# Performance work log

Measured on AMD Instinct MI355X. Metric: run time of the kernel, lower is better.

## Reference

```python
import jax, jax.numpy as jnp
import numpy as np

B, S, D_MODEL, HEAD, D_KV = 8, 1024, 1024, 16, 64


def setup_inputs() -> dict:
    key = jax.random.key(0)
    ks = jax.random.split(key, 10)
    std = 1.0 / np.sqrt(D_MODEL)
    inp = {
        "queries": jax.random.normal(ks[0], (B, S, D_MODEL), jnp.float32),
        "keys": jax.random.normal(ks[1], (B, S, D_MODEL), jnp.float32),
        "values": jax.random.normal(ks[2], (B, S, D_MODEL), jnp.float32),
        "group_prob": jax.random.uniform(ks[3], (B, 1, S, S), jnp.float32),
        "attention_mask": jax.random.randint(ks[4], (B, 1, S, S), 0, 2, jnp.int32),
        "Wq": jax.random.normal(ks[5], (HEAD * D_KV, D_MODEL), jnp.float32) * std,
        "bq": jnp.zeros((HEAD * D_KV,), jnp.float32),
        "Wk": jax.random.normal(ks[6], (HEAD * D_KV, D_MODEL), jnp.float32) * std,
        "bk": jnp.zeros((HEAD * D_KV,), jnp.float32),
        "Wv": jax.random.normal(ks[7], (HEAD * D_KV, D_MODEL), jnp.float32) * std,
        "bv": jnp.zeros((HEAD * D_KV,), jnp.float32),
    }
    return inp


def reference(queries, keys, values, group_prob, attention_mask, Wq, bq, Wk, bk, Wv, bv):
    b, nq = queries.shape[:2]
    # QKV projections -> [b, head, seq, d_kv]
    q = (queries @ Wq.T + bq).reshape(b, nq, HEAD, D_KV).transpose(0, 2, 1, 3)
    k = (keys @ Wk.T + bk).reshape(b, -1, HEAD, D_KV).transpose(0, 2, 1, 3)
    v = (values @ Wv.T + bv).reshape(b, -1, HEAD, D_KV).transpose(0, 2, 1, 3)
    # scaled scores [b, head, nq, nk]
    att = jnp.einsum("bhqd,bhkd->bhqk", q, k) / np.sqrt(D_KV).astype(np.float32)
    # NOTE: the original torch code calls att.masked_fill(...) (out-of-place)
    # and discards the result, so attention_mask has no effect. Replicated here.
    att = jax.nn.softmax(att, axis=-1)
    att = att * group_prob  # post-softmax group scaling (breaks fused SDPA)
    out = jnp.einsum("bhqk,bhkd->bhqd", att, v)
    return out.transpose(0, 2, 1, 3).reshape(b, nq, HEAD * D_KV)
```

## Files before the change

### kernel.cpp

```cpp
#include <hip/hip_runtime.h>

#define B_SZ 8
#define S_SZ 1024
#define DM   1024
#define NH   16
#define DK   64

typedef __bf16 bf16;
typedef __bf16 bf16x8 __attribute__((ext_vector_type(8)));
typedef float  f32x4  __attribute__((ext_vector_type(4)));

__device__ __forceinline__ f32x4 mfma16x16x32(bf16x8 a, bf16x8 b, f32x4 c) {
    return __builtin_amdgcn_mfma_f32_16x16x32_bf16(a, b, c, 0, 0, 0);
}

typedef const __attribute__((address_space(1))) void* gptr_t;
typedef __attribute__((address_space(3))) void*       sptr_t;
__device__ __forceinline__ void async_cp16(const void* g, void* s) {
    __builtin_amdgcn_global_load_lds((gptr_t)g, (sptr_t)s, 16, 0, 0);
}

__global__ __launch_bounds__(256)
void cvt_kernel(const float* __restrict__ x0, const float* __restrict__ x1,
                const float* __restrict__ x2, const float* __restrict__ w0,
                const float* __restrict__ w1, const float* __restrict__ w2,
                bf16* __restrict__ xb, bf16* __restrict__ wb)
{
    const int z = blockIdx.y;
    const float* src;
    bf16* dst;
    int n;
    if (z < 3) {
        src = (z == 0) ? x0 : (z == 1) ? x1 : x2;
        dst = xb + (size_t)z * (8u * 1024 * 1024);
        n = 8 * 1024 * 1024;
    } else {
        const int w = z - 3;
        src = (w == 0) ? w0 : (w == 1) ? w1 : w2;
        dst = wb + (size_t)w * (1024 * 1024);
        n = 1024 * 1024;
    }
    const int idx = (blockIdx.x * 256 + threadIdx.x) * 8;
    if (idx >= n) return;
    const float4 a = *(const float4*)(src + idx);
    const float4 c = *(const float4*)(src + idx + 4);
    union { bf16 h[8]; uint4 u; } pk;
    pk.h[0] = (bf16)a.x; pk.h[1] = (bf16)a.y; pk.h[2] = (bf16)a.z; pk.h[3] = (bf16)a.w;
    pk.h[4] = (bf16)c.x; pk.h[5] = (bf16)c.y; pk.h[6] = (bf16)c.z; pk.h[7] = (bf16)c.w;
    *(uint4*)(dst + idx) = pk.u;
}

__global__ __launch_bounds__(256)
void cvt_gp_kernel(const float* __restrict__ gp, bf16* __restrict__ gpb)
{
    const int idx = (blockIdx.x * 256 + threadIdx.x) * 8;
    const float4 a = *(const float4*)(gp + idx);
    const float4 c = *(const float4*)(gp + idx + 4);
    union { bf16 h[8]; uint4 u; } pk;
    pk.h[0] = (bf16)a.x; pk.h[1] = (bf16)a.y; pk.h[2] = (bf16)a.z; pk.h[3] = (bf16)a.w;
    pk.h[4] = (bf16)c.x; pk.h[5] = (bf16)c.y; pk.h[6] = (bf16)c.z; pk.h[7] = (bf16)c.w;
    *(uint4*)(gpb + idx) = pk.u;
}

__global__ __launch_bounds__(256, 2)
void qkv_gemm(const bf16* __restrict__ xb, const bf16* __restrict__ wb,
              const float* __restrict__ bq, const float* __restrict__ bk,
              const float* __restrict__ bv,
              bf16* __restrict__ qb, bf16* __restrict__ kb,
              bf16* __restrict__ vb)
{
    const int z = blockIdx.z;
    const bf16* A  = xb + (size_t)z * (8u * 1024 * 1024);
    const bf16* Bm = wb + (size_t)z * (1024 * 1024);
    const float* bias = (z == 0) ? bq : (z == 1) ? bk : bv;

    __shared__ bf16 Ash[128 * 64];
    __shared__ bf16 Bsh[128 * 64];

    const int tid  = threadIdx.x;
    const int wid  = tid >> 6;
    const int lane = tid & 63;
    const int quad = lane >> 4;
    const int l16  = lane & 15;
    const int wm   = wid >> 1, wn = wid & 1;
    const int bm   = blockIdx.x, bn = blockIdx.y;

    f32x4 acc[4][4] = {};

    for (int k0 = 0; k0 < DM; k0 += 64) {
        __syncthreads();
        #pragma unroll
        for (int i = 0; i < 4; ++i) {
            const int e   = (i * 256 + tid) * 8;
            const int row = e >> 6;
            const int c   = ((e >> 3) & 7) ^ (row & 7);
            async_cp16(A  + (size_t)(bm * 128 + row) * DM + k0 + c * 8, &Ash[e]);
            async_cp16(Bm + (size_t)(bn * 128 + row) * DM + k0 + c * 8, &Bsh[e]);
        }
        __syncthreads();

        #pragma unroll
        for (int ks = 0; ks < 2; ++ks) {
            bf16x8 af[4], bfr[4];
            #pragma unroll
            for (int mi = 0; mi < 4; ++mi) {
                const int row = wm * 64 + mi * 16 + l16;
                af[mi] = *(const bf16x8*)&Ash[row * 64 + (((ks * 4 + quad) ^ (l16 & 7)) << 3)];
            }
            #pragma unroll
            for (int ni = 0; ni < 4; ++ni) {
                const int row = wn * 64 + ni * 16 + l16;
                bfr[ni] = *(const bf16x8*)&Bsh[row * 64 + (((ks * 4 + quad) ^ (l16 & 7)) << 3)];
            }
            #pragma unroll
            for (int mi = 0; mi < 4; ++mi)
                #pragma unroll
                for (int ni = 0; ni < 4; ++ni)
                    acc[mi][ni] = mfma16x16x32(af[mi], bfr[ni], acc[mi][ni]);
        }
    }

    #pragma unroll
    for (int ni = 0; ni < 4; ++ni) {
        const int n    = bn * 128 + wn * 64 + ni * 16 + l16;
        const float bv_ = bias[n];
        const int h = n >> 6, d = n & 63;
        #pragma unroll
        for (int mi = 0; mi < 4; ++mi) {
            const int m0 = bm * 128 + wm * 64 + mi * 16 + quad * 4;
            const int b  = m0 >> 10;
            const int s0 = m0 & 1023;
            if (z == 2) {
                union { bf16 h4[4]; uint2 u; } pk;
                #pragma unroll
                for (int r = 0; r < 4; ++r) pk.h4[r] = (bf16)(acc[mi][ni][r] + bv_);
                *(uint2*)(vb + ((size_t)((b * NH + h) * DK + d)) * S_SZ + s0) = pk.u;
            } else {
                bf16* dst      = (z == 0) ? qb : kb;
                const float sc = (z == 0) ? 0.125f : 1.0f;
                #pragma unroll
                for (int r = 0; r < 4; ++r)
                    dst[((size_t)(b * NH + h) * S_SZ + (s0 + r)) * DK + d] =
                        (bf16)((acc[mi][ni][r] + bv_) * sc);
            }
        }
    }
}

__global__ __launch_bounds__(256, 3)
void attn_kernel(const bf16* __restrict__ qb, const bf16* __restrict__ kb,
                 const bf16* __restrict__ vb, const bf16* __restrict__ gpb,
                 float* __restrict__ out)
{
    __shared__ bf16 Ksh[128 * 64];
    __shared__ bf16 Vsh[64 * 128];
    __shared__ bf16 Psh[4][16 * 136];
    __shared__ float Lsh[4][16];

    const int tid  = threadIdx.x;
    const int wid  = tid >> 6;
    const int lane = tid & 63;
    const int quad = lane >> 4;
    const int l16  = lane & 15;

    const int bh = blockIdx.x;
    const int qt = blockIdx.y;
    const int b  = bh >> 4;
    const int h  = bh & (NH - 1);
    const int q0 = qt * 64 + wid * 16;

    const bf16* qr = qb + ((size_t)bh * S_SZ + q0 + l16) * DK;
    const bf16x8 qf0 = *(const bf16x8*)(qr + quad * 8);
    const bf16x8 qf1 = *(const bf16x8*)(qr + 32 + quad * 8);

    f32x4 acc[4] = {};
    float lpart = 0.0f;

    const bf16* gpq = gpb + ((size_t)b * S_SZ + q0 + l16) * S_SZ;

    for (int kt = 0; kt < S_SZ / 128; ++kt) {
        __syncthreads();
        #pragma unroll
        for (int i = 0; i < 4; ++i) {
            const int e   = (i * 256 + tid) * 8;
            const int row = e >> 6;
            const int c   = ((e >> 3) & 7) ^ (row & 7);
            async_cp16(kb + (size_t)bh * (S_SZ * DK) + (size_t)(kt * 128 + row) * DK + c * 8,
                       &Ksh[e]);
        }
        #pragma unroll
        for (int i = 0; i < 4; ++i) {
            const int e   = (i * 256 + tid) * 8;
            const int row = e >> 7;
            const int c   = ((e >> 3) & 15) ^ (row & 15);
            async_cp16(vb + ((size_t)bh * DK + row) * S_SZ + kt * 128 + c * 8, &Vsh[e]);
        }
        ushort4 gpl[8];
        #pragma unroll
        for (int nb = 0; nb < 8; ++nb)
            gpl[nb] = *(const ushort4*)(gpq + kt * 128 + nb * 16 + quad * 4);
        __syncthreads();

        f32x4 sc[8];
        #pragma unroll
        for (int nb = 0; nb < 8; ++nb) {
            const int row = nb * 16 + l16;
            const bf16x8 kf0 = *(const bf16x8*)&Ksh[row * 64 + ((quad ^ (l16 & 7)) << 3)];
            const bf16x8 kf1 = *(const bf16x8*)&Ksh[row * 64 + (((4 + quad) ^ (l16 & 7)) << 3)];
            f32x4 s = {0.0f, 0.0f, 0.0f, 0.0f};
            s = mfma16x16x32(kf0, qf0, s);
            s = mfma16x16x32(kf1, qf1, s);
            sc[nb] = s;
        }

        #pragma unroll
        for (int nb = 0; nb < 8; ++nb) {
            union { bf16 h4[4]; uint2 u; } pk;
            const unsigned short* gu = (const unsigned short*)&gpl[nb];
            #pragma unroll
            for (int r = 0; r < 4; ++r) {
                const float pv = __expf(sc[nb][r]);
                lpart += pv;
                const float g = __uint_as_float(((unsigned)gu[r]) << 16);
                pk.h4[r] = (bf16)(pv * g);
            }
            *(uint2*)&Psh[wid][l16 * 136 + nb * 16 + quad * 4] = pk.u;
        }

        bf16x8 pf[4];
        #pragma unroll
        for (int j = 0; j < 4; ++j)
            pf[j] = *(const bf16x8*)&Psh[wid][l16 * 136 + j * 32 + quad * 8];
        #pragma unroll
        for (int ni = 0; ni < 4; ++ni) {
            const int vrow = ni * 16 + l16;
            #pragma unroll
            for (int j = 0; j < 4; ++j) {
                const bf16x8 vf = *(const bf16x8*)&Vsh[vrow * 128 + (((j * 4 + quad) ^ l16) << 3)];
                acc[ni] = mfma16x16x32(pf[j], vf, acc[ni]);
            }
        }
    }

    lpart += __shfl_xor(lpart, 16, 64);
    lpart += __shfl_xor(lpart, 32, 64);
    if (quad == 0) Lsh[wid][l16] = 1.0f / lpart;
    __syncthreads();

    #pragma unroll
    for (int r = 0; r < 4; ++r) {
        const float inv = Lsh[wid][quad * 4 + r];
        float* orow = out + ((size_t)b * S_SZ + q0 + quad * 4 + r) * DM + h * DK;
        #pragma unroll
        for (int ni = 0; ni < 4; ++ni)
            orow[ni * 16 + l16] = acc[ni][r] * inv;
    }
}

extern "C" void kernel_launch(void* const* d_in, const int* in_sizes, int n_in,
                              void* d_out, int out_size, void* d_ws, size_t ws_size,
                              hipStream_t stream) {
    const float* queries = (const float*)d_in[0];
    const float* keys    = (const float*)d_in[1];
    const float* values  = (const float*)d_in[2];
    const float* gp      = (const float*)d_in[3];
    const float* Wq = (const float*)d_in[5];
    const float* bq = (const float*)d_in[6];
    const float* Wk = (const float*)d_in[7];
    const float* bk = (const float*)d_in[8];
    const float* Wv = (const float*)d_in[9];
    const float* bv = (const float*)d_in[10];
    float* out = (float*)d_out;

    bf16* xb = (bf16*)d_ws;
    bf16* wb = xb + (size_t)3 * 8 * 1024 * 1024;
    bf16* qb = wb + (size_t)3 * 1024 * 1024;
    bf16* kb = qb + (size_t)B_SZ * NH * S_SZ * DK;
    bf16* vb = kb + (size_t)B_SZ * NH * S_SZ * DK;
    bf16* gpb = xb;
    (void)ws_size; (void)in_sizes; (void)n_in; (void)out_size;

    dim3 gc(4096, 6);
    cvt_kernel<<<gc, 256, 0, stream>>>(queries, keys, values, Wq, Wk, Wv, xb, wb);

    dim3 g1(64, 8, 3);
    qkv_gemm<<<g1, 256, 0, stream>>>(xb, wb, bq, bk, bv, qb, kb, vb);

    cvt_gp_kernel<<<dim3(4096), 256, 0, stream>>>(gp, gpb);

    dim3 g2(B_SZ * NH , S_SZ / 64 , 1);
    attn_kernel<<<g2, 256, 0, stream>>>(qb, kb, vb, gpb, out);
}
```

Before: 349.4 us.

## Register-prefetch next tiles in GEMM and attention; read fp32 group_prob directly

Replaces the async global-to-LDS copies in the QKV GEMM and attention kernels with register prefetch. Each iteration stores the previously loaded tile to LDS, issues the global loads for the next tile, and then waits only on LDS traffic before the barrier, so the next tile's loads overlap compute. It also drops the separate group_prob bf16 conversion kernel, and attention reads the fp32 group_prob directly, which doubles that read traffic inside attention but removes a launch plus a full write and re-read. The GEMM launch bounds are raised to 3 blocks per SM, which may increase register pressure.

```diff
diff --git a/kernel.cpp b/kernel.cpp
--- a/kernel.cpp
+++ b/kernel.cpp
@@ -14,10 +14,9 @@
     return __builtin_amdgcn_mfma_f32_16x16x32_bf16(a, b, c, 0, 0, 0);
 }
 
-typedef const __attribute__((address_space(1))) void* gptr_t;
-typedef __attribute__((address_space(3))) void*       sptr_t;
-__device__ __forceinline__ void async_cp16(const void* g, void* s) {
-    __builtin_amdgcn_global_load_lds((gptr_t)g, (sptr_t)s, 16, 0, 0);
+__device__ __forceinline__ void barrier_lds_only() {
+    __builtin_amdgcn_s_waitcnt(0xC07F);
+    __builtin_amdgcn_s_barrier();
 }
 
 __global__ __launch_bounds__(256)
@@ -50,19 +49,7 @@
     *(uint4*)(dst + idx) = pk.u;
 }
 
-__global__ __launch_bounds__(256)
-void cvt_gp_kernel(const float* __restrict__ gp, bf16* __restrict__ gpb)
-{
-    const int idx = (blockIdx.x * 256 + threadIdx.x) * 8;
-    const float4 a = *(const float4*)(gp + idx);
-    const float4 c = *(const float4*)(gp + idx + 4);
-    union { bf16 h[8]; uint4 u; } pk;
-    pk.h[0] = (bf16)a.x; pk.h[1] = (bf16)a.y; pk.h[2] = (bf16)a.z; pk.h[3] = (bf16)a.w;
-    pk.h[4] = (bf16)c.x; pk.h[5] = (bf16)c.y; pk.h[6] = (bf16)c.z; pk.h[7] = (bf16)c.w;
-    *(uint4*)(gpb + idx) = pk.u;
-}
-
-__global__ __launch_bounds__(256, 2)
+__global__ __launch_bounds__(256, 3)
 void qkv_gemm(const bf16* __restrict__ xb, const bf16* __restrict__ wb,
               const float* __restrict__ bq, const float* __restrict__ bk,
               const float* __restrict__ bv,
@@ -87,17 +74,29 @@
 
     f32x4 acc[4][4] = {};
 
-    for (int k0 = 0; k0 < DM; k0 += 64) {
-        __syncthreads();
+    uint4 ra[4], rb[4];
+    auto load_tiles = [&](int k0) {
         #pragma unroll
         for (int i = 0; i < 4; ++i) {
             const int e   = (i * 256 + tid) * 8;
             const int row = e >> 6;
             const int c   = ((e >> 3) & 7) ^ (row & 7);
-            async_cp16(A  + (size_t)(bm * 128 + row) * DM + k0 + c * 8, &Ash[e]);
-            async_cp16(Bm + (size_t)(bn * 128 + row) * DM + k0 + c * 8, &Bsh[e]);
-        }
+            ra[i] = *(const uint4*)(A  + (size_t)(bm * 128 + row) * DM + k0 + c * 8);
+            rb[i] = *(const uint4*)(Bm + (size_t)(bn * 128 + row) * DM + k0 + c * 8);
+        }
+    };
+    load_tiles(0);
+
+    for (int k0 = 0; k0 < DM; k0 += 64) {
         __syncthreads();
+        #pragma unroll
+        for (int i = 0; i < 4; ++i) {
+            const int e = (i * 256 + tid) * 8;
+            *(uint4*)&Ash[e] = ra[i];
+            *(uint4*)&Bsh[e] = rb[i];
+        }
+        load_tiles((k0 + 64) & (DM - 1));
+        barrier_lds_only();
 
         #pragma unroll
         for (int ks = 0; ks < 2; ++ks) {
@@ -149,7 +148,7 @@
 
 __global__ __launch_bounds__(256, 3)
 void attn_kernel(const bf16* __restrict__ qb, const bf16* __restrict__ kb,
-                 const bf16* __restrict__ vb, const bf16* __restrict__ gpb,
+                 const bf16* __restrict__ vb, const float* __restrict__ gp,
                  float* __restrict__ out)
 {
     __shared__ bf16 Ksh[128 * 64];
@@ -176,30 +175,43 @@
     f32x4 acc[4] = {};
     float lpart = 0.0f;
 
-    const bf16* gpq = gpb + ((size_t)b * S_SZ + q0 + l16) * S_SZ;
+    const float* gpq = gp + ((size_t)b * S_SZ + q0 + l16) * S_SZ;
+
+    uint4 kr[4], vr[4];
+    auto load_kv = [&](int kt) {
+        #pragma unroll
+        for (int i = 0; i < 4; ++i) {
+            const int e = (i * 256 + tid) * 8;
+            {
+                const int row = e >> 6;
+                const int c   = ((e >> 3) & 7) ^ (row & 7);
+                kr[i] = *(const uint4*)(kb + (size_t)bh * (S_SZ * DK)
+                            + (size_t)(kt * 128 + row) * DK + c * 8);
+            }
+            {
+                const int row = e >> 7;
+                const int c   = ((e >> 3) & 15) ^ (row & 15);
+                vr[i] = *(const uint4*)(vb + ((size_t)bh * DK + row) * S_SZ
+                            + kt * 128 + c * 8);
+            }
+        }
+    };
+    load_kv(0);
 
     for (int kt = 0; kt < S_SZ / 128; ++kt) {
         __syncthreads();
         #pragma unroll
         for (int i = 0; i < 4; ++i) {
-            const int e   = (i * 256 + tid) * 8;
-            const int row = e >> 6;
-            const int c   = ((e >> 3) & 7) ^ (row & 7);
-            async_cp16(kb + (size_t)bh * (S_SZ * DK) + (size_t)(kt * 128 + row) * DK + c * 8,
-                       &Ksh[e]);
-        }
-        #pragma unroll
-        for (int i = 0; i < 4; ++i) {
-            const int e   = (i * 256 + tid) * 8;
-            const int row = e >> 7;
-            const int c   = ((e >> 3) & 15) ^ (row & 15);
-            async_cp16(vb + ((size_t)bh * DK + row) * S_SZ + kt * 128 + c * 8, &Vsh[e]);
-        }
-        ushort4 gpl[8];
+            const int e = (i * 256 + tid) * 8;
+            *(uint4*)&Ksh[e] = kr[i];
+            *(uint4*)&Vsh[e] = vr[i];
+        }
+        load_kv((kt + 1) & 7);
+        float4 gpl[8];
         #pragma unroll
         for (int nb = 0; nb < 8; ++nb)
-            gpl[nb] = *(const ushort4*)(gpq + kt * 128 + nb * 16 + quad * 4);
-        __syncthreads();
+            gpl[nb] = *(const float4*)(gpq + kt * 128 + nb * 16 + quad * 4);
+        barrier_lds_only();
 
         f32x4 sc[8];
         #pragma unroll
@@ -216,13 +228,12 @@
         #pragma unroll
         for (int nb = 0; nb < 8; ++nb) {
             union { bf16 h4[4]; uint2 u; } pk;
-            const unsigned short* gu = (const unsigned short*)&gpl[nb];
+            const float* g4 = (const float*)&gpl[nb];
             #pragma unroll
             for (int r = 0; r < 4; ++r) {
                 const float pv = __expf(sc[nb][r]);
                 lpart += pv;
-                const float g = __uint_as_float(((unsigned)gu[r]) << 16);
-                pk.h4[r] = (bf16)(pv * g);
+                pk.h4[r] = (bf16)(pv * g4[r]);
             }
             *(uint2*)&Psh[wid][l16 * 136 + nb * 16 + quad * 4] = pk.u;
         }
@@ -277,7 +288,6 @@
     bf16* qb = wb + (size_t)3 * 1024 * 1024;
     bf16* kb = qb + (size_t)B_SZ * NH * S_SZ * DK;
     bf16* vb = kb + (size_t)B_SZ * NH * S_SZ * DK;
-    bf16* gpb = xb;
     (void)ws_size; (void)in_sizes; (void)n_in; (void)out_size;
 
     dim3 gc(4096, 6);
@@ -286,8 +296,6 @@
     dim3 g1(64, 8, 3);
     qkv_gemm<<<g1, 256, 0, stream>>>(xb, wb, bq, bk, bv, qb, kb, vb);
 
-    cvt_gp_kernel<<<dim3(4096), 256, 0, stream>>>(gp, gpb);
-
     dim3 g2(B_SZ * NH , S_SZ / 64 , 1);
-    attn_kernel<<<g2, 256, 0, stream>>>(qb, kb, vb, gpb, out);
-}
+    attn_kernel<<<g2, 256, 0, stream>>>(qb, kb, vb, gp, out);
+}
```

Measured after the change: 812.6 us. 133% more time.
